# Optimization experiments

Measured on AMD Instinct MI355X. Metric: run time of the kernel, lower is better.

## Reference

```python
import jax, jax.numpy as jnp
import numpy as np

NEG = -1e30  # stand-in for -inf that keeps gradients finite
EPS = 1e-7   # keras.backend.epsilon()


def _ctc_loss(y_true, y_pred):
    # y_true: [B, L] int labels (values < C-1); y_pred: [B, T, C] probabilities.
    # Faithful to keras ctc_batch_cost -> tf1 ctc_loss: log(p+eps) is passed as
    # 'logits'; tf1 ctc_loss applies softmax internally (=> log_softmax here)
    # and uses blank index = C-1. input_length=T, label_length=L for all rows.
    B, T, C = y_pred.shape
    L = y_true.shape[1]
    blank = C - 1
    S = 2 * L + 1

    logp = jax.nn.log_softmax(jnp.log(y_pred + EPS), axis=-1)  # [B, T, C]

    # blank-interleaved extended label sequence: [blank, l0, blank, l1, ..., blank]
    ext = jnp.full((B, S), blank, dtype=jnp.int32).at[:, 1::2].set(
        y_true.astype(jnp.int32))  # [B, S]

    # gather per-state emission log-probs: lp_ext[b, t, s] = logp[b, t, ext[b, s]]
    idx = jnp.broadcast_to(ext[:, None, :], (B, T, S))
    lp_ext = jnp.take_along_axis(logp, idx, axis=2)  # [B, T, S]

    # skip (s-2) transition allowed when state is non-blank and differs from s-2
    ext_m2 = jnp.pad(ext[:, :-2], ((0, 0), (2, 0)), constant_values=-1)
    allow_skip = (ext != blank) & (ext != ext_m2)  # [B, S]

    alpha0 = (jnp.full((B, S), NEG, dtype=lp_ext.dtype)
              .at[:, 0].set(lp_ext[:, 0, 0])
              .at[:, 1].set(lp_ext[:, 0, 1]))

    def step(alpha, lp_t):
        a1 = alpha
        a2 = jnp.pad(alpha[:, :-1], ((0, 0), (1, 0)), constant_values=NEG)
        a3 = jnp.where(allow_skip,
                       jnp.pad(alpha[:, :-2], ((0, 0), (2, 0)), constant_values=NEG),
                       NEG)
        m = jnp.maximum(jnp.maximum(a1, a2), a3)
        alpha_new = m + jnp.log(jnp.exp(a1 - m) + jnp.exp(a2 - m) + jnp.exp(a3 - m)) + lp_t
        return alpha_new, None

    # scan over time steps 1..T-1 (time-major emission slices)
    alpha_T, _ = jax.lax.scan(step, alpha0, jnp.transpose(lp_ext, (1, 0, 2))[1:])
    loss = -jnp.logaddexp(alpha_T[:, S - 1], alpha_T[:, S - 2])  # [B]
    return loss[:, None]  # [B, 1], matching tf.expand_dims(..., 1)


def setup_inputs() -> dict:
    key = jax.random.key(0)
    k1, k2 = jax.random.split(key)
    B, T, C, L = 256, 1024, 256, 128
    y_true = jax.random.randint(k1, (B, L), 0, C - 1, dtype=jnp.int64)
    y_pred = jax.random.uniform(k2, (B, T, C), dtype=jnp.float32)
    return {"y_true": y_true, "y_pred": y_pred}


def reference(y_true, y_pred):
    # The keras layer returns y_pred and registers the loss via add_loss;
    # the loss is the computation of interest, so return it.
    return _ctc_loss(y_true, y_pred)
```

## Files before the change

### kernel.cpp

```cpp
#include <hip/hip_runtime.h>


#define B_DIM 256
#define T_DIM 1024
#define C_DIM 256
#define L_DIM 128
#define EPSF  (1e-7f)
#define CEPSF (256.0f * 1e-7f)
#define LN2F  (0.6931471805599453f)

__global__ __launch_bounds__(256) void row_stats_kernel(const float* __restrict__ yp,
                                                        float2* __restrict__ sm) {
    const int row  = (blockIdx.x << 2) + (threadIdx.x >> 6);
    const int lane = threadIdx.x & 63;
    const float4* rb = (const float4*)(yp + (size_t)row * C_DIM);
    float4 v = rb[lane];
    float e0 = v.x + EPSF, e1 = v.y + EPSF, e2 = v.z + EPSF, e3 = v.w + EPSF;
    float s  = v.x + v.y + v.z + v.w;
    float mx = fmaxf(fmaxf(e0, e1), fmaxf(e2, e3));
    #pragma unroll
    for (int d = 1; d < 64; d <<= 1) {
        s  += __shfl_xor(s, d, 64);
        mx  = fmaxf(mx, __shfl_xor(mx, d, 64));
    }
    if (lane == 0) {
        float invsum = 1.0f / (s + CEPSF);
        float tm = mx * invsum;
        int   M  = (__float_as_int(tm) >> 23) - 127;
        float srow = invsum * __int_as_float((127 - M) << 23);
        sm[row] = make_float2(srow, (float)M);
    }
}

__global__ __launch_bounds__(64) void ctc_dp_kernel(const int* __restrict__ yt,
                                                    const float* __restrict__ yp,
                                                    const float2* __restrict__ sm,
                                                    float* __restrict__ out)
{
    const int b = blockIdx.x, lane = threadIdx.x;
    const float* base = yp + (size_t)b * (T_DIM * C_DIM);
    const int* lab = yt + b * L_DIM;
    const int lab1 = lab[2 * lane];
    const int lab3 = lab[2 * lane + 1];
    const int labm = (lane == 0) ? -1 : lab[2 * lane - 1];
    const float sk1 = (lab1 != labm) ? 1.0f : 0.0f;
    const float sk3 = (lab3 != lab1) ? 1.0f : 0.0f;
    const float* p1p = base + lab1;
    const float* p3p = base + lab3;
    const float* pBp = base + (C_DIM - 1);
    const float2* smp = sm + b * T_DIM;
    const int  bpaddr = ((lane - 1) & 63) << 2;
    const bool l0 = (lane == 0);

    float r1[16], r3[16], rB[16];
    float2 rs[16];
#pragma unroll
    for (int u = 0; u < 16; ++u) {
        r1[u] = p1p[(size_t)u * C_DIM];
        r3[u] = p3p[(size_t)u * C_DIM];
        rB[u] = pBp[(size_t)u * C_DIM];
        rs[u] = smp[u];
    }

    float Mtot = 0.0f, Rtot = 0.0f;
    float c1, c3, cB, n1l, n3l, nB;
    float a0, a1, a2 = 0.0f, a3 = 0.0f, a4 = 0.0f;

#define LPL(S, o1, o3, oB) do {                 \
        float s_ = rs[S].x; Mtot += rs[S].y;    \
        (o1) = (r1[S] + EPSF) * s_;             \
        (o3) = (r3[S] + EPSF) * s_;             \
        (oB) = (rB[S] + EPSF) * s_; } while (0)

    { float i1, i3, iB; LPL(0, i1, i3, iB);
      a0 = l0 ? iB : 0.0f; a1 = l0 ? i1 : 0.0f; }
    LPL(1, c1, c3, cB);
    LPL(2, n1l, n3l, nB);
    int previ = __builtin_amdgcn_ds_bpermute(bpaddr, __float_as_int(a3));

    float m = 1.0f, w = 1.0f, s1f = 1.0f, s2f = 1.0f;

#define STEP(T_, SPF_, S2_, DOPF_, DOLP_, APPLY_) do {                     \
        float prev = l0 ? 0.0f : __int_as_float(previ);                    \
        if (APPLY_) { prev *= s1f; prev *= s2f;                            \
            a0 *= s1f; a1 *= s1f; a2 *= s1f; a3 *= s1f; a4 *= s1f;         \
            a0 *= s2f; a1 *= s2f; a2 *= s2f; a3 *= s2f; a4 *= s2f; }       \
        float x3 = (a3 + a2 + sk3 * a1) * c3;                              \
        previ = __builtin_amdgcn_ds_bpermute(bpaddr, __float_as_int(x3));  \
        float x0 = (a0 + prev) * cB;                                       \
        float x1 = (a1 + a0 + sk1 * prev) * c1;                            \
        float x2 = (a2 + a1) * cB;                                         \
        float x4 = (a4 + a3) * cB;                                         \
        a0 = x0; a1 = x1; a2 = x2; a3 = x3; a4 = x4;                       \
        if (DOPF_) { const size_t o_ = (size_t)((T_) + 15) * C_DIM;        \
            r1[SPF_] = p1p[o_]; r3[SPF_] = p3p[o_]; rB[SPF_] = pBp[o_];    \
            rs[SPF_] = smp[(T_) + 15]; }                                   \
        c1 = n1l; c3 = n3l; cB = nB;                                       \
        if (DOLP_) { LPL(S2_, n1l, n3l, nB); }                             \
    } while (0)

#define STAGES(K_)                                                          \
        if ((K_) == 0)  { m = fmaxf(fmaxf(a0, a1), fmaxf(fmaxf(a2, a3), a4)); \
                          w = __shfl_xor(m, 1, 64); }                       \
        if ((K_) == 2)  { m = fmaxf(m, w); w = __shfl_xor(m, 2, 64); }      \
        if ((K_) == 4)  { m = fmaxf(m, w); w = __shfl_xor(m, 4, 64); }      \
        if ((K_) == 6)  { m = fmaxf(m, w); w = __shfl_xor(m, 8, 64); }      \
        if ((K_) == 8)  { m = fmaxf(m, w); w = __shfl_xor(m, 16, 64); }     \
        if ((K_) == 10) { m = fmaxf(m, w); w = __shfl_xor(m, 32, 64); }     \
        if ((K_) == 12) { m = fmaxf(m, w);                                  \
                          int E  = (__float_as_int(m) >> 23) - 127;         \
                          int sh = 60 - E;                                  \
                          Rtot -= (float)sh;                                \
                          int sh1 = sh >> 1, sh2 = sh - sh1;                \
                          s1f = __int_as_float((sh1 + 127) << 23);          \
                          s2f = __int_as_float((sh2 + 127) << 23); }

#pragma unroll
    for (int k = 1; k <= 15; ++k) {
        STEP(k, (k - 1) & 15, (k + 2) & 15, 1, 1, 0);
    }

    for (int t0 = 16; t0 <= 992; t0 += 16) {
#pragma unroll
        for (int k = 0; k < 16; ++k) {
            STAGES(k)
            STEP(t0 + k, (k + 15) & 15, (k + 2) & 15, 1, 1, (k == 13));
        }
    }

    {
        const int t0 = 1008;
#pragma unroll
        for (int k = 0; k < 16; ++k) {
            STAGES(k)
            STEP(t0 + k, (k + 15) & 15, (k + 2) & 15, (k == 0), (k <= 13), (k == 13));
        }
    }

    if (lane == 63) {
        float v = a3 + a4;
        out[b] = -(log2f(v) + Mtot + Rtot) * LN2F;
    }
#undef STEP
#undef STAGES
#undef LPL
}

extern "C" void kernel_launch(void* const* d_in, const int* in_sizes, int n_in,
                              void* d_out, int out_size, void* d_ws, size_t ws_size,
                              hipStream_t stream) {
    const int*   yt = (const int*)d_in[0];
    const float* yp = (const float*)d_in[1];
    float* out = (float*)d_out;
    float2* sm = (float2*)d_ws;
    (void)in_sizes; (void)n_in; (void)out_size; (void)ws_size;
    row_stats_kernel<<<dim3((B_DIM * T_DIM) / 4), dim3(256), 0, stream>>>(yp, sm);
    ctc_dp_kernel<<<dim3(B_DIM), dim3(64), 0, stream>>>(yt, yp, sm, out);
}
```

Measured before the change: 491.5 us.

## Pre-gather label emissions into compact per-row buffer for the DP kernel

The row-statistics kernel now normalizes each row itself and, through LDS, gathers the scaled probabilities for all 128 labels plus the blank and exponent into a contiguous 132-float row in the workspace. The DP kernel then streams coalesced float2 loads from this compact buffer instead of doing scattered 4-byte gathers across full 256-class rows of the input. This takes scattered global reads off the latency-bound serial recurrence. The cost is extra writes in the first kernel and a larger workspace (B*T*132 floats).

```diff
diff --git a/kernel.cpp b/kernel.cpp
--- a/kernel.cpp
+++ b/kernel.cpp
@@ -5,16 +5,21 @@
 #define T_DIM 1024
 #define C_DIM 256
 #define L_DIM 128
+#define ROWF  132
 #define EPSF  (1e-7f)
 #define CEPSF (256.0f * 1e-7f)
 #define LN2F  (0.6931471805599453f)
 
-__global__ __launch_bounds__(256) void row_stats_kernel(const float* __restrict__ yp,
-                                                        float2* __restrict__ sm) {
-    const int row  = (blockIdx.x << 2) + (threadIdx.x >> 6);
+__global__ __launch_bounds__(256) void row_gather_kernel(const int* __restrict__ yt,
+                                                         const float* __restrict__ yp,
+                                                         float* __restrict__ cw) {
+    const int w    = threadIdx.x >> 6;
     const int lane = threadIdx.x & 63;
-    const float4* rb = (const float4*)(yp + (size_t)row * C_DIM);
-    float4 v = rb[lane];
+    const int row  = (blockIdx.x << 2) + w;
+    const int b    = row >> 10;
+    __shared__ float lds[4][C_DIM];
+
+    const float4 v = ((const float4*)(yp + (size_t)row * C_DIM))[lane];
     float e0 = v.x + EPSF, e1 = v.y + EPSF, e2 = v.z + EPSF, e3 = v.w + EPSF;
     float s  = v.x + v.y + v.z + v.w;
     float mx = fmaxf(fmaxf(e0, e1), fmaxf(e2, e3));
@@ -23,54 +28,52 @@
         s  += __shfl_xor(s, d, 64);
         mx  = fmaxf(mx, __shfl_xor(mx, d, 64));
     }
-    if (lane == 0) {
-        float invsum = 1.0f / (s + CEPSF);
-        float tm = mx * invsum;
-        int   M  = (__float_as_int(tm) >> 23) - 127;
-        float srow = invsum * __int_as_float((127 - M) << 23);
-        sm[row] = make_float2(srow, (float)M);
-    }
+    const float invsum = 1.0f / (s + CEPSF);
+    const float tm = mx * invsum;
+    const int   M  = (__float_as_int(tm) >> 23) - 127;
+    const float srow = invsum * __int_as_float((127 - M) << 23);
+    e0 *= srow; e1 *= srow; e2 *= srow; e3 *= srow;
+
+    *(float4*)&lds[w][lane << 2] = make_float4(e0, e1, e2, e3);
+    const int2 lp = ((const int2*)(yt + ((size_t)b << 7)))[lane];
+    __syncthreads();
+
+    float* rb = cw + (size_t)row * ROWF;
+    ((float2*)rb)[lane] = make_float2(lds[w][lp.x], lds[w][lp.y]);
+    if (lane == 63)
+        ((float2*)rb)[64] = make_float2(e3, (float)M);
 }
 
 __global__ __launch_bounds__(64) void ctc_dp_kernel(const int* __restrict__ yt,
-                                                    const float* __restrict__ yp,
-                                                    const float2* __restrict__ sm,
+                                                    const float* __restrict__ cw,
                                                     float* __restrict__ out)
 {
     const int b = blockIdx.x, lane = threadIdx.x;
-    const float* base = yp + (size_t)b * (T_DIM * C_DIM);
+    const float* base = cw + (size_t)b * (T_DIM * ROWF);
     const int* lab = yt + b * L_DIM;
     const int lab1 = lab[2 * lane];
     const int lab3 = lab[2 * lane + 1];
     const int labm = (lane == 0) ? -1 : lab[2 * lane - 1];
     const float sk1 = (lab1 != labm) ? 1.0f : 0.0f;
     const float sk3 = (lab3 != lab1) ? 1.0f : 0.0f;
-    const float* p1p = base + lab1;
-    const float* p3p = base + lab3;
-    const float* pBp = base + (C_DIM - 1);
-    const float2* smp = sm + b * T_DIM;
+    const float2* pcl = (const float2*)base + lane;
+    const float2* pbm = (const float2*)base + 64;
     const int  bpaddr = ((lane - 1) & 63) << 2;
     const bool l0 = (lane == 0);
 
-    float r1[16], r3[16], rB[16];
-    float2 rs[16];
+    float2 rc[16], rm[16];
 #pragma unroll
-    for (int u = 0; u < 16; ++u) {
-        r1[u] = p1p[(size_t)u * C_DIM];
-        r3[u] = p3p[(size_t)u * C_DIM];
-        rB[u] = pBp[(size_t)u * C_DIM];
-        rs[u] = smp[u];
-    }
+    for (int u = 0; u < 16; ++u) { rc[u] = pcl[u * 66]; rm[u] = pbm[u * 66]; }
 
     float Mtot = 0.0f, Rtot = 0.0f;
     float c1, c3, cB, n1l, n3l, nB;
     float a0, a1, a2 = 0.0f, a3 = 0.0f, a4 = 0.0f;
 
 #define LPL(S, o1, o3, oB) do {                 \
-        float s_ = rs[S].x; Mtot += rs[S].y;    \
-        (o1) = (r1[S] + EPSF) * s_;             \
-        (o3) = (r3[S] + EPSF) * s_;             \
-        (oB) = (rB[S] + EPSF) * s_; } while (0)
+        Mtot += rm[S].y;                        \
+        (o1) = rc[S].x;                         \
+        (o3) = rc[S].y;                         \
+        (oB) = rm[S].x; } while (0)
 
     { float i1, i3, iB; LPL(0, i1, i3, iB);
       a0 = l0 ? iB : 0.0f; a1 = l0 ? i1 : 0.0f; }
@@ -92,9 +95,8 @@
         float x2 = (a2 + a1) * cB;                                         \
         float x4 = (a4 + a3) * cB;                                         \
         a0 = x0; a1 = x1; a2 = x2; a3 = x3; a4 = x4;                       \
-        if (DOPF_) { const size_t o_ = (size_t)((T_) + 15) * C_DIM;        \
-            r1[SPF_] = p1p[o_]; r3[SPF_] = p3p[o_]; rB[SPF_] = pBp[o_];    \
-            rs[SPF_] = smp[(T_) + 15]; }                                   \
+        if (DOPF_) { const int o_ = ((T_) + 15) * 66;                      \
+            rc[SPF_] = pcl[o_]; rm[SPF_] = pbm[o_]; }                      \
         c1 = n1l; c3 = n3l; cB = nB;                                       \
         if (DOLP_) { LPL(S2_, n1l, n3l, nB); }                             \
     } while (0)
@@ -152,8 +154,8 @@
     const int*   yt = (const int*)d_in[0];
     const float* yp = (const float*)d_in[1];
     float* out = (float*)d_out;
-    float2* sm = (float2*)d_ws;
+    float* cw = (float*)d_ws;
     (void)in_sizes; (void)n_in; (void)out_size; (void)ws_size;
-    row_stats_kernel<<<dim3((B_DIM * T_DIM) / 4), dim3(256), 0, stream>>>(yp, sm);
-    ctc_dp_kernel<<<dim3(B_DIM), dim3(64), 0, stream>>>(yt, yp, sm, out);
+    row_gather_kernel<<<dim3((B_DIM * T_DIM) / 4), dim3(256), 0, stream>>>(yt, yp, cw);
+    ctc_dp_kernel<<<dim3(B_DIM), dim3(64), 0, stream>>>(yt, cw, out);
 }
```

New measurement: 485.4 us. No clear change (-1.2%).
